# Kernel optimization log

Measured on AMD Instinct MI355X. Metric: run time of the kernel, lower is better.

## Reference

```python
import jax, jax.numpy as jnp
import numpy as np

NPOINT, K = 1024, 16
BN_EPS = 1e-5


def farthest_point_sample(xyz, npoint):
    # xyz: [B, N, 3]. Deterministic start at index 0 (torch version uses randint).
    B, N, _ = xyz.shape

    def step(carry, _):
        distance, farthest = carry
        centroid = jnp.take_along_axis(xyz, farthest[:, None, None], axis=1)  # [B,1,3]
        dist = jnp.sum((xyz - centroid) ** 2, axis=-1)  # [B,N]
        distance = jnp.minimum(distance, dist)
        nxt = jnp.argmax(distance, axis=-1)
        return (distance, nxt), farthest

    init = (jnp.full((B, N), 1e10, dtype=xyz.dtype), jnp.zeros((B,), dtype=jnp.int32))
    _, cents = jax.lax.scan(step, init, None, length=npoint)
    return jnp.transpose(cents)  # [B, npoint]


def knn_idx(k, xyz, new_xyz):
    # squared distances [B,S,N] via ||a||^2 + ||b||^2 - 2 a.b (avoids [B,S,N,3] blowup)
    d = (jnp.sum(new_xyz ** 2, -1)[:, :, None]
         + jnp.sum(xyz ** 2, -1)[:, None, :]
         - 2.0 * jnp.einsum('bsc,bnc->bsn', new_xyz, xyz))
    _, idx = jax.lax.top_k(-d, k)  # k smallest distances
    return idx


def gather_points(points, idx):
    # points: [B,N,C], idx: [B,...] -> [B,...,C]
    return jax.vmap(lambda p, i: p[i])(points, idx)


def bn_train(x, gamma, beta):
    # BatchNorm1d in train mode: batch statistics, biased variance
    m = jnp.mean(x, axis=0)
    v = jnp.var(x, axis=0)
    return gamma * (x - m) * jax.lax.rsqrt(v + BN_EPS) + beta


def setup_inputs() -> dict:
    key = jax.random.key(0)
    ks = jax.random.split(key, 16)
    B, N, CIN, COUT = 8, 4096, 64, 128
    cin3 = CIN + 3          # 67
    ec = int(cin3 * 2.0)    # 134 (expand_ratio=2, hidden_ch arg is unused by InvResMLP)
    s = 0.05
    return {
        'xyz': jax.random.normal(ks[0], (B, N, 3), jnp.float32),
        'pts': jax.random.normal(ks[1], (B, N, CIN), jnp.float32),
        'fc1_w': jax.random.normal(ks[2], (cin3, ec), jnp.float32) * s,
        'fc1_b': jnp.zeros((ec,), jnp.float32),
        'bn1_g': jnp.ones((ec,), jnp.float32),
        'bn1_b': jnp.zeros((ec,), jnp.float32),
        'fc2_w': jax.random.normal(ks[3], (ec, ec), jnp.float32) * s,
        'fc2_b': jnp.zeros((ec,), jnp.float32),
        'bn2_g': jnp.ones((ec,), jnp.float32),
        'bn2_b': jnp.zeros((ec,), jnp.float32),
        'fc3_w': jax.random.normal(ks[4], (ec, COUT), jnp.float32) * s,
        'fc3_b': jnp.zeros((COUT,), jnp.float32),
        'bn3_g': jnp.ones((COUT,), jnp.float32),
        'bn3_b': jnp.zeros((COUT,), jnp.float32),
        'sc_w': jax.random.normal(ks[5], (cin3, COUT), jnp.float32) * s,
        'sc_b': jnp.zeros((COUT,), jnp.float32),
        'scbn_g': jnp.ones((COUT,), jnp.float32),
        'scbn_b': jnp.zeros((COUT,), jnp.float32),
    }


def reference(xyz, pts, fc1_w, fc1_b, bn1_g, bn1_b, fc2_w, fc2_b, bn2_g, bn2_b,
              fc3_w, fc3_b, bn3_g, bn3_b, sc_w, sc_b, scbn_g, scbn_b):
    # --- local_group: FPS + kNN grouping ---
    cent = farthest_point_sample(xyz, NPOINT)          # [B,S]
    new_xyz = gather_points(xyz, cent)                 # [B,S,3]
    idx = knn_idx(K, xyz, new_xyz)                     # [B,S,K]
    grouped_xyz = gather_points(xyz, idx)              # [B,S,K,3]
    grouped_pts = gather_points(pts, idx)              # [B,S,K,C]
    grouped_xyz_norm = grouped_xyz - new_xyz[:, :, None, :]
    x = jnp.concatenate([grouped_xyz_norm, grouped_pts], axis=-1)  # [B,S,K,C+3]

    # --- InvResMLP (pointwise, train-mode BN, dropout as identity) ---
    B, S, Kk, C = x.shape
    x = x.reshape(B * S * Kk, C)
    sc = bn_train(x @ sc_w + sc_b, scbn_g, scbn_b)
    h = jax.nn.relu(bn_train(x @ fc1_w + fc1_b, bn1_g, bn1_b))
    h = jax.nn.relu(bn_train(h @ fc2_w + fc2_b, bn2_g, bn2_b))
    h = bn_train(h @ fc3_w + fc3_b, bn3_g, bn3_b)
    h = jax.nn.relu(h + sc)
    feats = h.reshape(B, S, Kk, -1)

    new_pts = jnp.max(feats, axis=2)                   # [B,S,out_ch]
    return new_xyz, new_pts
```

## Files before the change

kernel.cpp:

```cpp
#include <hip/hip_runtime.h>
#include <cstdint>
#include <cstddef>

typedef short short8 __attribute__((ext_vector_type(8)));
typedef float f32x4 __attribute__((ext_vector_type(4)));

#define B_   8
#define N_   4096
#define S_   1024
#define K_   16
#define M_   131072
#define CIN_ 64

__device__ inline float bf2f(unsigned short u) {
    unsigned int v = ((unsigned int)u) << 16;
    return __builtin_bit_cast(float, v);
}
__device__ inline unsigned short f2bf(float f) {
    unsigned int u = __builtin_bit_cast(unsigned int, f);
    unsigned int lsb = (u >> 16) & 1u;
    u += 0x7fffu + lsb;
    return (unsigned short)(u >> 16);
}

template<int CTRL>
__device__ inline unsigned long long dpp_max(unsigned long long k) {
    unsigned lo = (unsigned)k, hi = (unsigned)(k >> 32);
    unsigned olo = (unsigned)__builtin_amdgcn_update_dpp(0, (int)lo, CTRL, 0xF, 0xF, true);
    unsigned ohi = (unsigned)__builtin_amdgcn_update_dpp(0, (int)hi, CTRL, 0xF, 0xF, true);
    unsigned long long ok = ((unsigned long long)ohi << 32) | (unsigned long long)olo;
    return ok > k ? ok : k;
}

__global__ __launch_bounds__(256) void fps_kernel(const float* __restrict__ xyz,
                                                  float* __restrict__ outxyz)
{
    __shared__ float px_s[N_], py_s[N_], pz_s[N_];
    __shared__ float sOut[S_ * 3];
    __shared__ unsigned long long sK[2][4];
    int b = blockIdx.x;
    const float* xb = xyz + (size_t)b * N_ * 3;
    int t = threadIdx.x;
    int w = t >> 6, l = t & 63;
    const int NP = 16;
    float px[NP], py[NP], pz[NP], dst[NP];
#pragma unroll
    for (int i = 0; i < NP; i++) {
        int p = i * 256 + t;
        px[i] = xb[p * 3 + 0];
        py[i] = xb[p * 3 + 1];
        pz[i] = xb[p * 3 + 2];
        dst[i] = 1e10f;
        px_s[p] = px[i]; py_s[p] = py[i]; pz_s[p] = pz[i];
        asm volatile("" : "+v"(px[i]), "+v"(py[i]), "+v"(pz[i]));
    }
    __syncthreads();
    float cx = px_s[0], cy = py_s[0], cz = pz_s[0];
    for (int s = 0; s < S_; s++) {
        if (t == 0) { sOut[s * 3 + 0] = cx; sOut[s * 3 + 1] = cy; sOut[s * 3 + 2] = cz; }
        if (s == S_ - 1) break;
        float bd = -1.0f; int bp = 0;
#pragma unroll
        for (int i = 0; i < NP; i++) {
            float dx = __fsub_rn(px[i], cx);
            float dy = __fsub_rn(py[i], cy);
            float dz = __fsub_rn(pz[i], cz);
            float d  = __fadd_rn(__fadd_rn(__fmul_rn(dx, dx), __fmul_rn(dy, dy)),
                                 __fmul_rn(dz, dz));
            float nd = fminf(dst[i], d);
            dst[i] = nd;
            if (nd > bd) { bd = nd; bp = i * 256 + t; }
        }
        unsigned long long key =
            ((unsigned long long)__builtin_bit_cast(unsigned, bd) << 32) |
            (unsigned long long)(unsigned)(4095 - bp);
        key = dpp_max<0xB1>(key);
        key = dpp_max<0x4E>(key);
        key = dpp_max<0x141>(key);
        key = dpp_max<0x140>(key);
        key = dpp_max<0x142>(key);
        key = dpp_max<0x143>(key);
        int par = s & 1;
        if (l == 63) sK[par][w] = key;
        __syncthreads();
        unsigned long long k0 = sK[par][0], k1 = sK[par][1];
        unsigned long long k2 = sK[par][2], k3 = sK[par][3];
        unsigned long long ka = k0 > k1 ? k0 : k1;
        unsigned long long kb = k2 > k3 ? k2 : k3;
        unsigned long long g  = ka > kb ? ka : kb;
        int p = 4095 - (int)(g & 0xFFFu);
        cx = px_s[p]; cy = py_s[p]; cz = pz_s[p];
    }
    __syncthreads();
    float* ob = outxyz + (size_t)b * S_ * 3;
    for (int i = t; i < S_ * 3; i += 256) ob[i] = sOut[i];
}

__global__ void sqn_kernel(const float* __restrict__ xyz, float* __restrict__ sqn)
{
    int i = blockIdx.x * 256 + threadIdx.x;
    if (i >= B_ * N_) return;
    float x = xyz[i * 3 + 0], y = xyz[i * 3 + 1], z = xyz[i * 3 + 2];
    sqn[i] = __fadd_rn(__fadd_rn(__fmul_rn(x, x), __fmul_rn(y, y)), __fmul_rn(z, z));
}

__global__ __launch_bounds__(256) void knn_kernel(const float* __restrict__ xyz,
                                                  const float* __restrict__ sqn,
                                                  const float* __restrict__ newxyz,
                                                  int* __restrict__ idx)
{
    int w = threadIdx.x >> 6, l = threadIdx.x & 63;
    int q = blockIdx.x * 4 + w;
    int b = q >> 10;
    const float* xb = xyz + (size_t)b * N_ * 3;
    const float* sb = sqn + (size_t)b * N_;
    float qx = newxyz[(size_t)q * 3 + 0];
    float qy = newxyz[(size_t)q * 3 + 1];
    float qz = newxyz[(size_t)q * 3 + 2];
    float sa = __fadd_rn(__fadd_rn(__fmul_rn(qx, qx), __fmul_rn(qy, qy)), __fmul_rn(qz, qz));

    float d16[16]; int i16[16];
#pragma unroll
    for (int j = 0; j < 16; j++) { d16[j] = 3.0e38f; i16[j] = -1; }
    for (int i = 0; i < N_ / 64; i++) {
        int n = i * 64 + l;
        float bx = xb[n * 3 + 0], by = xb[n * 3 + 1], bz = xb[n * 3 + 2];
        float dot = __fmaf_rn(qz, bz, __fmaf_rn(qy, by, __fmul_rn(qx, bx)));
        float d = __fsub_rn(__fadd_rn(sa, sb[n]), __fmul_rn(2.0f, dot));
        if (d < d16[0]) {
            d16[0] = d; i16[0] = n;
#pragma unroll
            for (int j = 0; j < 15; j++) {
                if (d16[j] < d16[j + 1]) {
                    float td = d16[j]; d16[j] = d16[j + 1]; d16[j + 1] = td;
                    int   ti = i16[j]; i16[j] = i16[j + 1]; i16[j + 1] = ti;
                }
            }
        }
    }
    int* iq = idx + (size_t)q * 16;
#pragma unroll
    for (int r = 0; r < 16; r++) {
        float cd = d16[15]; int cn = i16[15];
#pragma unroll
        for (int off = 1; off < 64; off <<= 1) {
            float od = __shfl_xor(cd, off);
            int   on = __shfl_xor(cn, off);
            if (od < cd || (od == cd && on < cn)) { cd = od; cn = on; }
        }
        if (l == 0) iq[r] = cn;
        if (i16[15] == cn) {
#pragma unroll
            for (int j = 15; j >= 1; j--) { d16[j] = d16[j - 1]; i16[j] = i16[j - 1]; }
            d16[0] = 3.0e38f; i16[0] = -1;
        }
    }
}

__global__ void build_x(const float* __restrict__ xyz, const float* __restrict__ pts,
                        const float* __restrict__ newxyz, const int* __restrict__ idx,
                        unsigned short* __restrict__ X)
{
    int tid = blockIdx.x * 256 + threadIdx.x;
    int j = tid % 6;
    int r = tid / 6;
    float v[16];
#pragma unroll
    for (int e = 0; e < 16; e++) v[e] = 0.0f;
    if (j < 5) {
        int n = idx[r];
        int s = (r >> 4) & 1023;
        int b = r >> 14;
        const float* pr = pts + ((size_t)b * N_ + n) * CIN_;
        if (j == 0) {
#pragma unroll
            for (int c = 0; c < 3; c++)
                v[c] = xyz[((size_t)b * N_ + n) * 3 + c] - newxyz[((size_t)b * S_ + s) * 3 + c];
#pragma unroll
            for (int c = 3; c < 16; c++) v[c] = pr[c - 3];
        } else if (j == 4) {
#pragma unroll
            for (int c = 0; c < 3; c++) v[c] = pr[61 + c];
        } else {
            int base = j * 16 - 3;
#pragma unroll
            for (int c = 0; c < 16; c++) v[c] = pr[base + c];
        }
    }
    short8 lo, hi;
#pragma unroll
    for (int e = 0; e < 8; e++) { lo[e] = (short)f2bf(v[e]); hi[e] = (short)f2bf(v[8 + e]); }
    unsigned short* xp = X + (size_t)r * 96 + j * 16;
    *(short8*)xp = lo;
    *(short8*)(xp + 8) = hi;
}

__global__ void fill_wt(unsigned short* __restrict__ dst, const float* __restrict__ src,
                        int Kreal, int Nrows, int Nsrc, int KPAD)
{
    int tid = blockIdx.x * 256 + threadIdx.x;
    if (tid >= Nrows * KPAD) return;
    int row = tid / KPAD, k = tid % KPAD;
    float v = (k < Kreal && row < Nsrc) ? src[(size_t)k * Nsrc + row] : 0.0f;
    dst[tid] = f2bf(v);
}

template<int KPAD, int NF>
__global__ __launch_bounds__(256) void gemm_bn(
    const unsigned short* __restrict__ A, const unsigned short* __restrict__ Wt,
    unsigned short* __restrict__ Z1, int ld1, int n1real, float* sum1, float* sq1,
    unsigned short* __restrict__ Z2, int ld2, int n2real, float* sum2, float* sq2,
    int split)
{
    __shared__ unsigned short sA[128 * KPAD];
    __shared__ float sSt[NF * 32];
    int t = threadIdx.x;
    int r0 = blockIdx.x * 128;
    for (int i = t; i < NF * 32; i += 256) sSt[i] = 0.0f;
    {
        const uint4* ga = (const uint4*)(A + (size_t)r0 * KPAD);
        uint4* la = (uint4*)sA;
        const int CNT = 128 * KPAD * 2 / 16;
        for (int i = t; i < CNT; i += 256) la[i] = ga[i];
    }
    __syncthreads();
    int w = t >> 6, l = t & 63, lhi = l >> 4, llo = l & 15;
    f32x4 acc[2][NF];
#pragma unroll
    for (int m = 0; m < 2; m++)
#pragma unroll
        for (int n = 0; n < NF; n++) acc[m][n] = (f32x4){0.f, 0.f, 0.f, 0.f};
#pragma unroll
    for (int ks = 0; ks < KPAD / 32; ks++) {
        short8 bfr[NF];
#pragma unroll
        for (int n = 0; n < NF; n++)
            bfr[n] = *(const short8*)(Wt + (size_t)(n * 16 + llo) * KPAD + ks * 32 + lhi * 8);
#pragma unroll
        for (int m = 0; m < 2; m++) {
            short8 afr = *(const short8*)(sA + (w * 32 + m * 16 + llo) * KPAD + ks * 32 + lhi * 8);
#pragma unroll
            for (int n = 0; n < NF; n++)
                acc[m][n] = __builtin_amdgcn_mfma_f32_16x16x32_bf16(afr, bfr[n], acc[m][n], 0, 0, 0);
        }
    }
#pragma unroll
    for (int n = 0; n < NF; n++) {
        int c = n * 16 + llo;
        float ss = 0.f, sq = 0.f;
#pragma unroll
        for (int m = 0; m < 2; m++) {
#pragma unroll
            for (int j = 0; j < 4; j++) {
                float v = acc[m][n][j];
                int row = r0 + w * 32 + m * 16 + lhi * 4 + j;
                unsigned short hv = f2bf(v);
                if (c < split) Z1[(size_t)row * ld1 + c] = hv;
                else           Z2[(size_t)row * ld2 + (c - split)] = hv;
                ss += v; sq += v * v;
            }
        }
        ss += __shfl_xor(ss, 16); ss += __shfl_xor(ss, 32);
        sq += __shfl_xor(sq, 16); sq += __shfl_xor(sq, 32);
        if (l < 16) { atomicAdd(&sSt[c * 2], ss); atomicAdd(&sSt[c * 2 + 1], sq); }
    }
    __syncthreads();
    for (int c = t; c < NF * 16; c += 256) {
        float ss = sSt[c * 2], sq = sSt[c * 2 + 1];
        if (c < split) {
            if (c < n1real) { atomicAdd(&sum1[c], ss); atomicAdd(&sq1[c], sq); }
        } else {
            int cc = c - split;
            if (cc < n2real) { atomicAdd(&sum2[cc], ss); atomicAdd(&sq2[cc], sq); }
        }
    }
}

__global__ void bn_finalize(const float* __restrict__ sum, const float* __restrict__ sq,
                            const float* __restrict__ g, const float* __restrict__ bb,
                            float* __restrict__ a, float* __restrict__ c, int n)
{
    int i = blockIdx.x * 256 + threadIdx.x;
    if (i >= n) return;
    const float inv = 1.0f / (float)M_;
    float m = sum[i] * inv;
    float var = sq[i] * inv - m * m;
    float av = g[i] * rsqrtf(var + 1e-5f);
    a[i] = av;
    c[i] = bb[i] - av * m;
}

__global__ void norm_relu_v(const unsigned short* __restrict__ Z,
                            unsigned short* __restrict__ H,
                            const float* __restrict__ a, const float* __restrict__ c)
{
    int tid = blockIdx.x * 256 + threadIdx.x;
    int j = tid % 20;
    size_t r = (size_t)(tid / 20);
    int col0 = j * 8;
    short8 hv = {0, 0, 0, 0, 0, 0, 0, 0};
    if (col0 < 134) {
        short8 zv = *(const short8*)(Z + r * 144 + col0);
#pragma unroll
        for (int e = 0; e < 8; e++) {
            int col = col0 + e;
            float av = a[col], cv = c[col];
            float v = fmaxf(av * bf2f((unsigned short)zv[e]) + cv, 0.0f);
            hv[e] = (col < 134) ? (short)f2bf(v) : (short)0;
        }
    }
    *(short8*)(H + r * 160 + col0) = hv;
}

__global__ void final_kernel(const unsigned short* __restrict__ Z3,
                             const unsigned short* __restrict__ ZSC,
                             const float* __restrict__ a3, const float* __restrict__ c3,
                             const float* __restrict__ asc, const float* __restrict__ csc,
                             float* __restrict__ out)
{
    int tid = blockIdx.x * 256 + threadIdx.x;
    int bs = tid >> 4, ch0 = (tid & 15) * 8;
    float A3[8], C3[8], AS[8], CS[8], mx[8];
#pragma unroll
    for (int e = 0; e < 8; e++) {
        A3[e] = a3[ch0 + e]; C3[e] = c3[ch0 + e];
        AS[e] = asc[ch0 + e]; CS[e] = csc[ch0 + e];
        mx[e] = 0.0f;
    }
    const unsigned short* z3p = Z3 + (size_t)bs * 16 * 128 + ch0;
    const unsigned short* zsp = ZSC + (size_t)bs * 16 * 128 + ch0;
#pragma unroll
    for (int k = 0; k < 16; k++) {
        short8 z3 = *(const short8*)(z3p + (size_t)k * 128);
        short8 zs = *(const short8*)(zsp + (size_t)k * 128);
#pragma unroll
        for (int e = 0; e < 8; e++) {
            float y = fmaxf(A3[e] * bf2f((unsigned short)z3[e]) + C3[e]
                            + AS[e] * bf2f((unsigned short)zs[e]) + CS[e], 0.0f);
            mx[e] = fmaxf(mx[e], y);
        }
    }
    float* op = out + 24576 + (size_t)bs * 128 + ch0;
#pragma unroll
    for (int e = 0; e < 8; e++) op[e] = mx[e];
}

#define WS_STATS 0
#define WS_WT1   16384
#define WS_WT2   68608
#define WS_WT3   114688
#define WS_SQN   155648
#define WS_IDX   286720
#define WS_X     811008
#define WS_Z     25976832
#define WS_ZSC   63725568
#define WS_H     97280000

extern "C" void kernel_launch(void* const* d_in, const int* in_sizes, int n_in,
                              void* d_out, int out_size, void* d_ws, size_t ws_size,
                              hipStream_t stream)
{
    const float* xyz    = (const float*)d_in[0];
    const float* pts    = (const float*)d_in[1];
    const float* fc1_w  = (const float*)d_in[2];
    const float* bn1_g  = (const float*)d_in[4];
    const float* bn1_b  = (const float*)d_in[5];
    const float* fc2_w  = (const float*)d_in[6];
    const float* bn2_g  = (const float*)d_in[8];
    const float* bn2_b  = (const float*)d_in[9];
    const float* fc3_w  = (const float*)d_in[10];
    const float* bn3_g  = (const float*)d_in[12];
    const float* bn3_b  = (const float*)d_in[13];
    const float* sc_w   = (const float*)d_in[14];
    const float* scbn_g = (const float*)d_in[16];
    const float* scbn_b = (const float*)d_in[17];

    char* ws = (char*)d_ws;
    float* st = (float*)(ws + WS_STATS);
    float* bn1_sum = st + 0,    *bn1_sq = st + 134;
    float* bnsc_sum = st + 268, *bnsc_sq = st + 396;
    float* bn2_sum = st + 524,  *bn2_sq = st + 658;
    float* bn3_sum = st + 792,  *bn3_sq = st + 920;
    float* a1 = st + 1048, *c1 = st + 1182;
    float* a2 = st + 1316, *c2 = st + 1450;
    float* a3 = st + 1584, *c3 = st + 1712;
    float* asc = st + 1840, *csc = st + 1968;

    unsigned short* WT1 = (unsigned short*)(ws + WS_WT1);
    unsigned short* WT2 = (unsigned short*)(ws + WS_WT2);
    unsigned short* WT3 = (unsigned short*)(ws + WS_WT3);
    float* SQN = (float*)(ws + WS_SQN);
    int*   IDX = (int*)(ws + WS_IDX);
    unsigned short* X   = (unsigned short*)(ws + WS_X);
    unsigned short* Z   = (unsigned short*)(ws + WS_Z);
    unsigned short* ZSC = (unsigned short*)(ws + WS_ZSC);
    unsigned short* H   = (unsigned short*)(ws + WS_H);
    float* out = (float*)d_out;

    hipMemsetAsync(ws + WS_STATS, 0, 1048 * 4, stream);

    fill_wt<<<54, 256, 0, stream>>>(WT1, fc1_w, 67, 144, 134, 96);
    fill_wt<<<48, 256, 0, stream>>>(WT1 + 144 * 96, sc_w, 67, 128, 128, 96);
    fill_wt<<<90, 256, 0, stream>>>(WT2, fc2_w, 134, 144, 134, 160);
    fill_wt<<<80, 256, 0, stream>>>(WT3, fc3_w, 134, 128, 128, 160);

    fps_kernel<<<8, 256, 0, stream>>>(xyz, out);
    sqn_kernel<<<128, 256, 0, stream>>>(xyz, SQN);
    knn_kernel<<<2048, 256, 0, stream>>>(xyz, SQN, out, IDX);
    build_x<<<3072, 256, 0, stream>>>(xyz, pts, out, IDX, X);

    gemm_bn<96, 17><<<1024, 256, 0, stream>>>(X, WT1,
        Z, 144, 134, bn1_sum, bn1_sq,
        ZSC, 128, 128, bnsc_sum, bnsc_sq, 144);
    bn_finalize<<<1, 256, 0, stream>>>(bn1_sum, bn1_sq, bn1_g, bn1_b, a1, c1, 134);
    bn_finalize<<<1, 256, 0, stream>>>(bnsc_sum, bnsc_sq, scbn_g, scbn_b, asc, csc, 128);
    norm_relu_v<<<10240, 256, 0, stream>>>(Z, H, a1, c1);

    gemm_bn<160, 9><<<1024, 256, 0, stream>>>(H, WT2,
        Z, 144, 134, bn2_sum, bn2_sq,
        Z, 144, 0, bn2_sum, bn2_sq, 144);
    bn_finalize<<<1, 256, 0, stream>>>(bn2_sum, bn2_sq, bn2_g, bn2_b, a2, c2, 134);
    norm_relu_v<<<10240, 256, 0, stream>>>(Z, H, a2, c2);

    gemm_bn<160, 8><<<1024, 256, 0, stream>>>(H, WT3,
        Z, 128, 128, bn3_sum, bn3_sq,
        Z, 128, 0, bn3_sum, bn3_sq, 128);
    bn_finalize<<<1, 256, 0, stream>>>(bn3_sum, bn3_sq, bn3_g, bn3_b, a3, c3, 128);

    final_kernel<<<512, 256, 0, stream>>>(Z, ZSC, a3, c3, asc, csc, out);
}
```

Measured before the change: 1.124 ms.

## Fuse weight prep, sqnorm into FPS launch; fuse kNN with gather; fold BN finalize

```diff
diff --git a/kernel.cpp b/kernel.cpp
--- a/kernel.cpp
+++ b/kernel.cpp
@@ -4,6 +4,7 @@
 
 typedef short short8 __attribute__((ext_vector_type(8)));
 typedef float f32x4 __attribute__((ext_vector_type(4)));
+typedef unsigned long long u64x2 __attribute__((ext_vector_type(2)));
 
 #define B_   8
 #define N_   4096
@@ -32,18 +33,54 @@
     return ok > k ? ok : k;
 }
 
-__global__ __launch_bounds__(256) void fps_kernel(const float* __restrict__ xyz,
-                                                  float* __restrict__ outxyz)
+__global__ __launch_bounds__(256) void fps_aux_kernel(
+    const float* __restrict__ xyz, float* __restrict__ outxyz,
+    const float* __restrict__ fc1_w, const float* __restrict__ sc_w,
+    const float* __restrict__ fc2_w, const float* __restrict__ fc3_w,
+    unsigned short* __restrict__ WT1, unsigned short* __restrict__ WT2,
+    unsigned short* __restrict__ WT3, float* __restrict__ sqn)
 {
     __shared__ float px_s[N_], py_s[N_], pz_s[N_];
     __shared__ float sOut[S_ * 3];
     __shared__ unsigned long long sK[2][4];
+    int t = threadIdx.x;
+
+    if (blockIdx.x >= 8) {
+        int aux = blockIdx.x - 8;
+#pragma unroll
+        for (int ch = 0; ch < 10; ch++) {
+            int idx = (aux * 10 + ch) * 256 + t;
+            if (idx < 13824) {
+                int row = idx / 96, k = idx % 96;
+                WT1[idx] = f2bf((k < 67 && row < 134) ? fc1_w[k * 134 + row] : 0.0f);
+            } else if (idx < 26112) {
+                int j = idx - 13824;
+                int row = j / 96, k = j % 96;
+                WT1[13824 + j] = f2bf((k < 67) ? sc_w[k * 128 + row] : 0.0f);
+            } else if (idx < 49152) {
+                int j = idx - 26112;
+                int row = j / 160, k = j % 160;
+                WT2[j] = f2bf((k < 134 && row < 134) ? fc2_w[k * 134 + row] : 0.0f);
+            } else if (idx < 69632) {
+                int j = idx - 49152;
+                int row = j / 160, k = j % 160;
+                WT3[j] = f2bf((k < 134) ? fc3_w[k * 128 + row] : 0.0f);
+            } else {
+                int i = idx - 69632;
+                float x = xyz[i * 3 + 0], y = xyz[i * 3 + 1], z = xyz[i * 3 + 2];
+                sqn[i] = __fadd_rn(__fadd_rn(__fmul_rn(x, x), __fmul_rn(y, y)),
+                                   __fmul_rn(z, z));
+            }
+        }
+        return;
+    }
+
     int b = blockIdx.x;
     const float* xb = xyz + (size_t)b * N_ * 3;
-    int t = threadIdx.x;
     int w = t >> 6, l = t & 63;
     const int NP = 16;
     float px[NP], py[NP], pz[NP], dst[NP];
+    int klo_[NP];
 #pragma unroll
     for (int i = 0; i < NP; i++) {
         int p = i * 256 + t;
@@ -51,6 +88,7 @@
         py[i] = xb[p * 3 + 1];
         pz[i] = xb[p * 3 + 2];
         dst[i] = 1e10f;
+        klo_[i] = 4095 - p;
         px_s[p] = px[i]; py_s[p] = py[i]; pz_s[p] = pz[i];
         asm volatile("" : "+v"(px[i]), "+v"(py[i]), "+v"(pz[i]));
     }
@@ -59,7 +97,7 @@
     for (int s = 0; s < S_; s++) {
         if (t == 0) { sOut[s * 3 + 0] = cx; sOut[s * 3 + 1] = cy; sOut[s * 3 + 2] = cz; }
         if (s == S_ - 1) break;
-        float bd = -1.0f; int bp = 0;
+        float bd = -1.0f; int bk = 0;
 #pragma unroll
         for (int i = 0; i < NP; i++) {
             float dx = __fsub_rn(px[i], cx);
@@ -69,11 +107,11 @@
                                  __fmul_rn(dz, dz));
             float nd = fminf(dst[i], d);
             dst[i] = nd;
-            if (nd > bd) { bd = nd; bp = i * 256 + t; }
+            if (nd > bd) { bd = nd; bk = klo_[i]; }
         }
         unsigned long long key =
             ((unsigned long long)__builtin_bit_cast(unsigned, bd) << 32) |
-            (unsigned long long)(unsigned)(4095 - bp);
+            (unsigned long long)(unsigned)bk;
         key = dpp_max<0xB1>(key);
         key = dpp_max<0x4E>(key);
         key = dpp_max<0x141>(key);
@@ -83,10 +121,10 @@
         int par = s & 1;
         if (l == 63) sK[par][w] = key;
         __syncthreads();
-        unsigned long long k0 = sK[par][0], k1 = sK[par][1];
-        unsigned long long k2 = sK[par][2], k3 = sK[par][3];
-        unsigned long long ka = k0 > k1 ? k0 : k1;
-        unsigned long long kb = k2 > k3 ? k2 : k3;
+        u64x2 kA = *(u64x2*)&sK[par][0];
+        u64x2 kB = *(u64x2*)&sK[par][2];
+        unsigned long long ka = kA[0] > kA[1] ? kA[0] : kA[1];
+        unsigned long long kb = kB[0] > kB[1] ? kB[0] : kB[1];
         unsigned long long g  = ka > kb ? ka : kb;
         int p = 4095 - (int)(g & 0xFFFu);
         cx = px_s[p]; cy = py_s[p]; cz = pz_s[p];
@@ -96,19 +134,13 @@
     for (int i = t; i < S_ * 3; i += 256) ob[i] = sOut[i];
 }
 
-__global__ void sqn_kernel(const float* __restrict__ xyz, float* __restrict__ sqn)
-{
-    int i = blockIdx.x * 256 + threadIdx.x;
-    if (i >= B_ * N_) return;
-    float x = xyz[i * 3 + 0], y = xyz[i * 3 + 1], z = xyz[i * 3 + 2];
-    sqn[i] = __fadd_rn(__fadd_rn(__fmul_rn(x, x), __fmul_rn(y, y)), __fmul_rn(z, z));
-}
-
-__global__ __launch_bounds__(256) void knn_kernel(const float* __restrict__ xyz,
-                                                  const float* __restrict__ sqn,
-                                                  const float* __restrict__ newxyz,
-                                                  int* __restrict__ idx)
-{
+__global__ __launch_bounds__(256) void knn_build(const float* __restrict__ xyz,
+                                                 const float* __restrict__ sqn,
+                                                 const float* __restrict__ newxyz,
+                                                 const float* __restrict__ pts,
+                                                 unsigned short* __restrict__ X)
+{
+    __shared__ int sNbr[4][16];
     int w = threadIdx.x >> 6, l = threadIdx.x & 63;
     int q = blockIdx.x * 4 + w;
     int b = q >> 10;
@@ -138,7 +170,6 @@
             }
         }
     }
-    int* iq = idx + (size_t)q * 16;
 #pragma unroll
     for (int r = 0; r < 16; r++) {
         float cd = d16[15]; int cn = i16[15];
@@ -148,69 +179,47 @@
             int   on = __shfl_xor(cn, off);
             if (od < cd || (od == cd && on < cn)) { cd = od; cn = on; }
         }
-        if (l == 0) iq[r] = cn;
+        if (l == 0) sNbr[w][r] = cn;
         if (i16[15] == cn) {
 #pragma unroll
             for (int j = 15; j >= 1; j--) { d16[j] = d16[j - 1]; i16[j] = i16[j - 1]; }
             d16[0] = 3.0e38f; i16[0] = -1;
         }
     }
-}
-
-__global__ void build_x(const float* __restrict__ xyz, const float* __restrict__ pts,
-                        const float* __restrict__ newxyz, const int* __restrict__ idx,
-                        unsigned short* __restrict__ X)
-{
-    int tid = blockIdx.x * 256 + threadIdx.x;
-    int j = tid % 6;
-    int r = tid / 6;
-    float v[16];
-#pragma unroll
-    for (int e = 0; e < 16; e++) v[e] = 0.0f;
-    if (j < 5) {
-        int n = idx[r];
-        int s = (r >> 4) & 1023;
-        int b = r >> 14;
-        const float* pr = pts + ((size_t)b * N_ + n) * CIN_;
-        if (j == 0) {
-#pragma unroll
-            for (int c = 0; c < 3; c++)
-                v[c] = xyz[((size_t)b * N_ + n) * 3 + c] - newxyz[((size_t)b * S_ + s) * 3 + c];
-#pragma unroll
-            for (int c = 3; c < 16; c++) v[c] = pr[c - 3];
-        } else if (j == 4) {
-#pragma unroll
-            for (int c = 0; c < 3; c++) v[c] = pr[61 + c];
-        } else {
-            int base = j * 16 - 3;
-#pragma unroll
-            for (int c = 0; c < 16; c++) v[c] = pr[base + c];
-        }
-    }
-    short8 lo, hi;
-#pragma unroll
-    for (int e = 0; e < 8; e++) { lo[e] = (short)f2bf(v[e]); hi[e] = (short)f2bf(v[8 + e]); }
-    unsigned short* xp = X + (size_t)r * 96 + j * 16;
-    *(short8*)xp = lo;
-    *(short8*)(xp + 8) = hi;
-}
-
-__global__ void fill_wt(unsigned short* __restrict__ dst, const float* __restrict__ src,
-                        int Kreal, int Nrows, int Nsrc, int KPAD)
-{
-    int tid = blockIdx.x * 256 + threadIdx.x;
-    if (tid >= Nrows * KPAD) return;
-    int row = tid / KPAD, k = tid % KPAD;
-    float v = (k < Kreal && row < Nsrc) ? src[(size_t)k * Nsrc + row] : 0.0f;
-    dst[tid] = f2bf(v);
+    __syncthreads();
+    int row = l >> 2, seg = l & 3;
+    int n = sNbr[w][row];
+    const float* pr = pts + ((size_t)b * N_ + n) * CIN_;
+    const float* xr = xyz + ((size_t)b * N_ + n) * 3;
+    float v[24];
+#pragma unroll
+    for (int e = 0; e < 24; e++) {
+        int c = seg * 24 + e;
+        float val;
+        if (c == 0)      val = xr[0] - qx;
+        else if (c == 1) val = xr[1] - qy;
+        else if (c == 2) val = xr[2] - qz;
+        else if (c < 67) val = pr[c - 3];
+        else             val = 0.0f;
+        v[e] = val;
+    }
+    short8 s0, s1, s2;
+#pragma unroll
+    for (int e = 0; e < 8; e++) {
+        s0[e] = (short)f2bf(v[e]);
+        s1[e] = (short)f2bf(v[8 + e]);
+        s2[e] = (short)f2bf(v[16 + e]);
+    }
+    unsigned short* xp = X + ((size_t)q * 16 + row) * 96 + seg * 24;
+    *(short8*)xp = s0;
+    *(short8*)(xp + 8) = s1;
+    *(short8*)(xp + 16) = s2;
 }
 
 template<int KPAD, int NF>
 __global__ __launch_bounds__(256) void gemm_bn(
     const unsigned short* __restrict__ A, const unsigned short* __restrict__ Wt,
-    unsigned short* __restrict__ Z1, int ld1, int n1real, float* sum1, float* sq1,
-    unsigned short* __restrict__ Z2, int ld2, int n2real, float* sum2, float* sq2,
-    int split)
+    unsigned short* __restrict__ Z1, int ld1, int n1real, float* sum1, float* sq1)
 {
     __shared__ unsigned short sA[128 * KPAD];
     __shared__ float sSt[NF * 32];
@@ -254,9 +263,7 @@
             for (int j = 0; j < 4; j++) {
                 float v = acc[m][n][j];
                 int row = r0 + w * 32 + m * 16 + lhi * 4 + j;
-                unsigned short hv = f2bf(v);
-                if (c < split) Z1[(size_t)row * ld1 + c] = hv;
-                else           Z2[(size_t)row * ld2 + (c - split)] = hv;
+                Z1[(size_t)row * ld1 + c] = f2bf(v);
                 ss += v; sq += v * v;
             }
         }
@@ -266,35 +273,35 @@
     }
     __syncthreads();
     for (int c = t; c < NF * 16; c += 256) {
-        float ss = sSt[c * 2], sq = sSt[c * 2 + 1];
-        if (c < split) {
-            if (c < n1real) { atomicAdd(&sum1[c], ss); atomicAdd(&sq1[c], sq); }
-        } else {
-            int cc = c - split;
-            if (cc < n2real) { atomicAdd(&sum2[cc], ss); atomicAdd(&sq2[cc], sq); }
-        }
-    }
-}
-
-__global__ void bn_finalize(const float* __restrict__ sum, const float* __restrict__ sq,
-                            const float* __restrict__ g, const float* __restrict__ bb,
-                            float* __restrict__ a, float* __restrict__ c, int n)
-{
-    int i = blockIdx.x * 256 + threadIdx.x;
-    if (i >= n) return;
-    const float inv = 1.0f / (float)M_;
-    float m = sum[i] * inv;
-    float var = sq[i] * inv - m * m;
-    float av = g[i] * rsqrtf(var + 1e-5f);
-    a[i] = av;
-    c[i] = bb[i] - av * m;
-}
-
-__global__ void norm_relu_v(const unsigned short* __restrict__ Z,
-                            unsigned short* __restrict__ H,
-                            const float* __restrict__ a, const float* __restrict__ c)
-{
-    int tid = blockIdx.x * 256 + threadIdx.x;
+        if (c < n1real) {
+            atomicAdd(&sum1[c], sSt[c * 2]);
+            atomicAdd(&sq1[c], sSt[c * 2 + 1]);
+        }
+    }
+}
+
+__global__ __launch_bounds__(256) void norm_relu_v(const unsigned short* __restrict__ Z,
+                                                   unsigned short* __restrict__ H,
+                                                   const float* __restrict__ sum,
+                                                   const float* __restrict__ sq,
+                                                   const float* __restrict__ g,
+                                                   const float* __restrict__ bb)
+{
+    __shared__ float sAC[272];
+    int t = threadIdx.x;
+    if (t < 136) {
+        float a = 0.0f, c = 0.0f;
+        if (t < 134) {
+            const float inv = 1.0f / (float)M_;
+            float m = sum[t] * inv;
+            float var = sq[t] * inv - m * m;
+            a = g[t] * rsqrtf(var + 1e-5f);
+            c = bb[t] - a * m;
+        }
+        sAC[2 * t] = a; sAC[2 * t + 1] = c;
+    }
+    __syncthreads();
+    int tid = blockIdx.x * 256 + t;
     int j = tid % 20;
     size_t r = (size_t)(tid / 20);
     int col0 = j * 8;
@@ -304,27 +311,40 @@
 #pragma unroll
         for (int e = 0; e < 8; e++) {
             int col = col0 + e;
-            float av = a[col], cv = c[col];
-            float v = fmaxf(av * bf2f((unsigned short)zv[e]) + cv, 0.0f);
+            float2 ac = *(float2*)&sAC[2 * col];
+            float v = fmaxf(ac.x * bf2f((unsigned short)zv[e]) + ac.y, 0.0f);
             hv[e] = (col < 134) ? (short)f2bf(v) : (short)0;
         }
     }
     *(short8*)(H + r * 160 + col0) = hv;
 }
 
-__global__ void final_kernel(const unsigned short* __restrict__ Z3,
-                             const unsigned short* __restrict__ ZSC,
-                             const float* __restrict__ a3, const float* __restrict__ c3,
-                             const float* __restrict__ asc, const float* __restrict__ csc,
-                             float* __restrict__ out)
-{
-    int tid = blockIdx.x * 256 + threadIdx.x;
+__global__ __launch_bounds__(256) void final_kernel(
+    const unsigned short* __restrict__ Z3, const unsigned short* __restrict__ ZSC,
+    const float* __restrict__ sum3, const float* __restrict__ sq3,
+    const float* __restrict__ g3, const float* __restrict__ b3,
+    const float* __restrict__ sumsc, const float* __restrict__ sqsc,
+    const float* __restrict__ gsc, const float* __restrict__ bsc,
+    float* __restrict__ out)
+{
+    __shared__ float sF[512];
+    int t = threadIdx.x;
+    if (t < 128) {
+        const float inv = 1.0f / (float)M_;
+        float m3 = sum3[t] * inv, v3 = sq3[t] * inv - m3 * m3;
+        float a3 = g3[t] * rsqrtf(v3 + 1e-5f), c3 = b3[t] - a3 * m3;
+        float ms = sumsc[t] * inv, vs = sqsc[t] * inv - ms * ms;
+        float as = gsc[t] * rsqrtf(vs + 1e-5f), cs = bsc[t] - as * ms;
+        sF[t * 4 + 0] = a3; sF[t * 4 + 1] = c3; sF[t * 4 + 2] = as; sF[t * 4 + 3] = cs;
+    }
+    __syncthreads();
+    int tid = blockIdx.x * 256 + t;
     int bs = tid >> 4, ch0 = (tid & 15) * 8;
     float A3[8], C3[8], AS[8], CS[8], mx[8];
 #pragma unroll
     for (int e = 0; e < 8; e++) {
-        A3[e] = a3[ch0 + e]; C3[e] = c3[ch0 + e];
-        AS[e] = asc[ch0 + e]; CS[e] = csc[ch0 + e];
+        f32x4 f = *(f32x4*)&sF[(ch0 + e) * 4];
+        A3[e] = f[0]; C3[e] = f[1]; AS[e] = f[2]; CS[e] = f[3];
         mx[e] = 0.0f;
     }
     const unsigned short* z3p = Z3 + (size_t)bs * 16 * 128 + ch0;
@@ -346,15 +366,14 @@
 }
 
 #define WS_STATS 0
-#define WS_WT1   16384
-#define WS_WT2   68608
-#define WS_WT3   114688
-#define WS_SQN   155648
-#define WS_IDX   286720
-#define WS_X     811008
-#define WS_Z     25976832
-#define WS_ZSC   63725568
-#define WS_H     97280000
+#define WS_WT1   8192
+#define WS_WT2   61440
+#define WS_WT3   108544
+#define WS_SQN   149760
+#define WS_X     281088
+#define WS_Z     25447424
+#define WS_ZSC   63196416
+#define WS_H     96751104
 
 extern "C" void kernel_launch(void* const* d_in, const int* in_sizes, int n_in,
                               void* d_out, int out_size, void* d_ws, size_t ws_size,
@@ -377,55 +396,36 @@
 
     char* ws = (char*)d_ws;
     float* st = (float*)(ws + WS_STATS);
-    float* bn1_sum = st + 0,    *bn1_sq = st + 134;
-    float* bnsc_sum = st + 268, *bnsc_sq = st + 396;
-    float* bn2_sum = st + 524,  *bn2_sq = st + 658;
-    float* bn3_sum = st + 792,  *bn3_sq = st + 920;
-    float* a1 = st + 1048, *c1 = st + 1182;
-    float* a2 = st + 1316, *c2 = st + 1450;
-    float* a3 = st + 1584, *c3 = st + 1712;
-    float* asc = st + 1840, *csc = st + 1968;
+    float* bn1_sum = st + 0,   *bn1_sq = st + 136;
+    float* bnsc_sum = st + 272, *bnsc_sq = st + 400;
+    float* bn2_sum = st + 528, *bn2_sq = st + 664;
+    float* bn3_sum = st + 800, *bn3_sq = st + 928;
 
     unsigned short* WT1 = (unsigned short*)(ws + WS_WT1);
     unsigned short* WT2 = (unsigned short*)(ws + WS_WT2);
     unsigned short* WT3 = (unsigned short*)(ws + WS_WT3);
     float* SQN = (float*)(ws + WS_SQN);
-    int*   IDX = (int*)(ws + WS_IDX);
     unsigned short* X   = (unsigned short*)(ws + WS_X);
     unsigned short* Z   = (unsigned short*)(ws + WS_Z);
     unsigned short* ZSC = (unsigned short*)(ws + WS_ZSC);
     unsigned short* H   = (unsigned short*)(ws + WS_H);
     float* out = (float*)d_out;
 
-    hipMemsetAsync(ws + WS_STATS, 0, 1048 * 4, stream);
-
-    fill_wt<<<54, 256, 0, stream>>>(WT1, fc1_w, 67, 144, 134, 96);
-    fill_wt<<<48, 256, 0, stream>>>(WT1 + 144 * 96, sc_w, 67, 128, 128, 96);
-    fill_wt<<<90, 256, 0, stream>>>(WT2, fc2_w, 134, 144, 134, 160);
-    fill_wt<<<80, 256, 0, stream>>>(WT3, fc3_w, 134, 128, 128, 160);
-
-    fps_kernel<<<8, 256, 0, stream>>>(xyz, out);
-    sqn_kernel<<<128, 256, 0, stream>>>(xyz, SQN);
-    knn_kernel<<<2048, 256, 0, stream>>>(xyz, SQN, out, IDX);
-    build_x<<<3072, 256, 0, stream>>>(xyz, pts, out, IDX, X);
-
-    gemm_bn<96, 17><<<1024, 256, 0, stream>>>(X, WT1,
-        Z, 144, 134, bn1_sum, bn1_sq,
-        ZSC, 128, 128, bnsc_sum, bnsc_sq, 144);
-    bn_finalize<<<1, 256, 0, stream>>>(bn1_sum, bn1_sq, bn1_g, bn1_b, a1, c1, 134);
-    bn_finalize<<<1, 256, 0, stream>>>(bnsc_sum, bnsc_sq, scbn_g, scbn_b, asc, csc, 128);
-    norm_relu_v<<<10240, 256, 0, stream>>>(Z, H, a1, c1);
-
-    gemm_bn<160, 9><<<1024, 256, 0, stream>>>(H, WT2,
-        Z, 144, 134, bn2_sum, bn2_sq,
-        Z, 144, 0, bn2_sum, bn2_sq, 144);
-    bn_finalize<<<1, 256, 0, stream>>>(bn2_sum, bn2_sq, bn2_g, bn2_b, a2, c2, 134);
-    norm_relu_v<<<10240, 256, 0, stream>>>(Z, H, a2, c2);
-
-    gemm_bn<160, 8><<<1024, 256, 0, stream>>>(H, WT3,
-        Z, 128, 128, bn3_sum, bn3_sq,
-        Z, 128, 0, bn3_sum, bn3_sq, 128);
-    bn_finalize<<<1, 256, 0, stream>>>(bn3_sum, bn3_sq, bn3_g, bn3_b, a3, c3, 128);
-
-    final_kernel<<<512, 256, 0, stream>>>(Z, ZSC, a3, c3, asc, csc, out);
-}
+    hipMemsetAsync(ws + WS_STATS, 0, 1056 * 4, stream);
+
+    fps_aux_kernel<<<48, 256, 0, stream>>>(xyz, out, fc1_w, sc_w, fc2_w, fc3_w,
+                                           WT1, WT2, WT3, SQN);
+    knn_build<<<2048, 256, 0, stream>>>(xyz, SQN, out, pts, X);
+
+    gemm_bn<96, 9><<<1024, 256, 0, stream>>>(X, WT1, Z, 144, 134, bn1_sum, bn1_sq);
+    gemm_bn<96, 8><<<1024, 256, 0, stream>>>(X, WT1 + 13824, ZSC, 128, 128, bnsc_sum, bnsc_sq);
+    norm_relu_v<<<10240, 256, 0, stream>>>(Z, H, bn1_sum, bn1_sq, bn1_g, bn1_b);
+
+    gemm_bn<160, 9><<<1024, 256, 0, stream>>>(H, WT2, Z, 144, 134, bn2_sum, bn2_sq);
+    norm_relu_v<<<10240, 256, 0, stream>>>(Z, H, bn2_sum, bn2_sq, bn2_g, bn2_b);
+
+    gemm_bn<160, 8><<<1024, 256, 0, stream>>>(H, WT3, Z, 128, 128, bn3_sum, bn3_sq);
+
+    final_kernel<<<512, 256, 0, stream>>>(Z, ZSC, bn3_sum, bn3_sq, bn3_g, bn3_b,
+                                          bnsc_sum, bnsc_sq, scbn_g, scbn_b, out);
+}
```

New measurement: 1.037 ms. 7.7% less time.
